# Performance work log

Measured on AMD Instinct MI355X. Metric: run time of the kernel, lower is better.

Reference implementation:

```python
import jax, jax.numpy as jnp
import numpy as np

B = 512       # batch
N = 64        # max_nodes
H = 256       # hidden_dim
LAT = 128     # latent_dim
HEADS = 4
HC = H // HEADS   # per-head channels (GATConv out_channels)
NF = 64       # node_features
L = 3         # num_dec_layers
R = 8         # lora_r
SCAL = 16.0 / R   # lora_alpha / r
NB = 4        # num_bond_types
SLOPE = 0.2   # GATConv leaky_relu negative slope


def setup_inputs() -> dict:
    key = jax.random.key(0)
    ks = jax.random.split(key, 21)
    f = lambda k, shape, s=0.05: jax.random.normal(k, shape, dtype=jnp.float32) * s
    Din = H + LAT  # GAT input dim = hidden + latent (concat)
    return {
        "z": jax.random.normal(ks[0], (B, LAT), dtype=jnp.float32),
        # z_to_nodes LoRALinear: latent -> hidden*max_nodes
        "z2n_w": f(ks[1], (H * N, LAT)), "z2n_b": f(ks[2], (H * N,)),
        "z2n_A": f(ks[3], (R, LAT)), "z2n_B": f(ks[4], (H * N, R)),
        # GATConv stacks (same Din every layer): lin weight, att_src, att_dst, bias
        "gat_W": f(ks[5], (L, HEADS * HC, Din)),
        "gat_asrc": f(ks[6], (L, HEADS, HC)),
        "gat_adst": f(ks[7], (L, HEADS, HC)),
        "gat_bias": f(ks[8], (L, H)),
        # node predictor LoRALinear: hidden -> node_features
        "node_w": f(ks[9], (NF, H)), "node_b": f(ks[10], (NF,)),
        "node_A": f(ks[11], (R, H)), "node_B": f(ks[12], (NF, R)),
        # adj predictor LoRALinear: 2*hidden -> 1
        "adj_w": f(ks[13], (1, 2 * H)), "adj_b": f(ks[14], (1,)),
        "adj_A": f(ks[15], (R, 2 * H)), "adj_B": f(ks[16], (1, R)),
        # bond type predictor LoRALinear: 2*hidden -> 4
        "bond_w": f(ks[17], (NB, 2 * H)), "bond_b": f(ks[18], (NB,)),
        "bond_A": f(ks[19], (R, 2 * H)), "bond_B": f(ks[20], (NB, R)),
    }


def _lora_w(W, A, Bm):
    # effective weight of LoRALinear (eval mode, dropout off): W + (alpha/r) * B @ A
    return W + SCAL * (Bm @ A)


def _forward(z, z2n_w, z2n_b, z2n_A, z2n_B, gat_W, gat_asrc, gat_adst, gat_bias,
             node_w, node_b, node_A, node_B, adj_w, adj_b, adj_A, adj_B,
             bond_w, bond_b, bond_A, bond_B):
    # z_to_nodes: LoRA linear + ReLU -> [B, N, H]
    x = jax.nn.relu(z @ _lora_w(z2n_w, z2n_A, z2n_B).T + z2n_b).reshape(B, N, H)
    z_bc = jnp.broadcast_to(z[:, None, :], (B, N, LAT))
    # Fully-connected graph (off-diagonal edges) + GATConv default self loops
    # => dense softmax attention over all N source nodes per target, per graph.
    for l in range(L):
        xc = jnp.concatenate([x, z_bc], axis=-1)                      # [B,N,H+LAT]
        Wr = gat_W[l].reshape(HEADS, HC, H + LAT)
        h = jnp.einsum('bnd,hcd->bnhc', xc, Wr)                        # [B,N,heads,HC]
        e_src = jnp.einsum('bnhc,hc->bnh', h, gat_asrc[l])             # source term
        e_dst = jnp.einsum('bnhc,hc->bnh', h, gat_adst[l])             # target term
        e = e_dst[:, :, None, :] + e_src[:, None, :, :]                # [B,i,j,heads]
        e = jnp.where(e > 0, e, SLOPE * e)                             # leaky_relu
        alpha = jax.nn.softmax(e, axis=2)                              # over sources j
        out = jnp.einsum('bijh,bjhc->bihc', alpha, h).reshape(B, N, H) + gat_bias[l]
        x = jax.nn.relu(out)
    # node reconstruction
    recon_nodes = x @ _lora_w(node_w, node_A, node_B).T + node_b       # [B,N,NF]
    # pairwise predictors: Linear(concat[h_i,h_j]) = W1 h_i + W2 h_j + b
    iu = jnp.triu(jnp.ones((N, N), dtype=bool), 1)
    Wa = _lora_w(adj_w, adj_A, adj_B)                                  # [1,2H]
    s1 = x @ Wa[:, :H].T                                               # [B,N,1]
    s2 = x @ Wa[:, H:].T
    Am = s1 + jnp.swapaxes(s2, 1, 2) + adj_b[0]                        # Am[i,j]=s1[i]+s2[j]
    adj_logits = jnp.where(iu, Am, jnp.where(iu.T, jnp.swapaxes(Am, 1, 2), 0.0))
    Wb = _lora_w(bond_w, bond_A, bond_B)                               # [NB,2H]
    t1 = x @ Wb[:, :H].T                                               # [B,N,NB]
    t2 = x @ Wb[:, H:].T
    Bm = t1[:, :, None, :] + t2[:, None, :, :] + bond_b                # [B,N,N,NB]
    bond_logits = jnp.where(iu[:, :, None], Bm,
                            jnp.where(iu.T[:, :, None], jnp.swapaxes(Bm, 1, 2), 0.0))
    return recon_nodes, adj_logits, bond_logits


def reference(z, z2n_w, z2n_b, z2n_A, z2n_B, gat_W, gat_asrc, gat_adst, gat_bias,
              node_w, node_b, node_A, node_B, adj_w, adj_b, adj_A, adj_B,
              bond_w, bond_b, bond_A, bond_B):
    return _forward(z, z2n_w, z2n_b, z2n_A, z2n_B, gat_W, gat_asrc, gat_adst, gat_bias,
                    node_w, node_b, node_A, node_B, adj_w, adj_b, adj_A, adj_B,
                    bond_w, bond_b, bond_A, bond_B)
```

## Files before the change

kernel.cpp:

```cpp
#include <hip/hip_runtime.h>


typedef float float4v __attribute__((ext_vector_type(4)));
typedef short short8v __attribute__((ext_vector_type(8)));

struct alignas(8) us4 { ushort x, y, z, w; };

#define ZA_OFF 0UL
#define HZ_OFF 4096UL
#define EZ_OFF 397312UL
#define XBF_U   819200UL
#define ZBF_U   9207808UL
#define GWBF_U  9273344UL
#define WZBF_U  9568256UL
#define PW_U    11665408UL
#define WST_U   11759616UL

__device__ inline ushort f2bf(float f) {
    uint u = __float_as_uint(f);
    uint r = (u + 0x7FFFu + ((u >> 16) & 1u)) >> 16;
    return (ushort)r;
}
__device__ inline float bf2f(ushort u) { return __uint_as_float(((uint)u) << 16); }

__device__ inline int xidx(int r, int cu) {
    int ch = cu >> 3;
    return r * 256 + (((ch ^ (r & 7))) << 3) + (cu & 7);
}

struct P3 { short8v b0, b1, b2; };
__device__ inline P3 loadP3(const ushort* pw, int lo, int hi, int kk) {
    P3 f;
    f.b0 = *(const short8v*)(pw + (size_t)(      lo)*256 + kk*32 + hi*8);
    f.b1 = *(const short8v*)(pw + (size_t)(16  + lo)*256 + kk*32 + hi*8);
    f.b2 = *(const short8v*)(pw + (size_t)(32  + lo)*256 + kk*32 + hi*8);
    return f;
}
struct P2 { short8v b3, b4; };
__device__ inline P2 loadP2(const ushort* pw, int lo, int hi, int kk) {
    P2 f;
    f.b3 = *(const short8v*)(pw + (size_t)(48 + lo)*256 + kk*32 + hi*8);
    f.b4 = *(const short8v*)(pw + (size_t)(64 + lo)*256 + kk*32 + hi*8);
    return f;
}

__device__ inline void gll(const ushort* src, ushort* dst) {
    __builtin_amdgcn_global_load_lds(
        (const __attribute__((address_space(1))) void*)src,
        (__attribute__((address_space(3))) void*)dst, 16, 0, 0);
}

__device__ inline void stageW(ushort* dstHead, const ushort* srcHead, int c0h, int ln) {
    if (c0h == 0) {
        gll(srcHead +        ln*8, dstHead);
        gll(srcHead +  512 + ln*8, dstHead + 512);
        gll(srcHead + 2048 + ln*8, dstHead + 2048);
    } else {
        gll(srcHead + 1024 + ln*8, dstHead + 1024);
        gll(srcHead + 1536 + ln*8, dstHead + 1536);
    }
}

__global__ __launch_bounds__(256) void k_setup(
    const float* __restrict__ z, const float* __restrict__ z2nA,
    const float* __restrict__ nodeW, const float* __restrict__ nodeA, const float* __restrict__ nodeB,
    const float* __restrict__ adjW, const float* __restrict__ adjA, const float* __restrict__ adjB,
    const float* __restrict__ bondW, const float* __restrict__ bondA, const float* __restrict__ bondB,
    const float* __restrict__ gatW, const float* __restrict__ z2nw,
    const float* __restrict__ asrcp, const float* __restrict__ adstp,
    float* __restrict__ wsf)
{
    ushort* wsu = (ushort*)wsf;
    int gid = blockIdx.x * 256 + threadIdx.x;
    if (gid < 4096) {
        int b = gid >> 3, r = gid & 7;
        const float* zp = z + (size_t)b * 128;
        const float* ap = z2nA + (size_t)r * 128;
        float s = 0.f;
        #pragma unroll 8
        for (int k = 0; k < 128; ++k) s += zp[k] * ap[k];
        wsf[ZA_OFF + gid] = s;
    } else if (gid < 24576) {
        int idx = gid - 4096;
        int r = idx >> 8, c = idx & 255;
        float v = 0.f;
        if (r < 64) {
            float s = 0.f;
            #pragma unroll
            for (int k = 0; k < 8; ++k) s += nodeB[r*8+k] * nodeA[k*256+c];
            v = nodeW[r*256+c] + 2.0f * s;
        } else if (r < 66) {
            int off = (r - 64) * 256 + c;
            float s = 0.f;
            #pragma unroll
            for (int k = 0; k < 8; ++k) s += adjB[k] * adjA[k*512+off];
            v = adjW[off] + 2.0f * s;
        } else if (r < 70) {
            int q = r - 66;
            float s = 0.f;
            #pragma unroll
            for (int k = 0; k < 8; ++k) s += bondB[q*8+k] * bondA[k*512+c];
            v = bondW[q*512+c] + 2.0f * s;
        } else if (r < 74) {
            int q = r - 70;
            float s = 0.f;
            #pragma unroll
            for (int k = 0; k < 8; ++k) s += bondB[q*8+k] * bondA[k*512+256+c];
            v = bondW[q*512+256+c] + 2.0f * s;
        }
        wsu[PW_U + idx] = f2bf(v);
    } else if (gid < 55296) {
        int idx = gid - 24576;
        int lkk = idx / 1280;
        int rem = idx - lkk * 1280;
        int head = rem / 320;
        int rem2 = rem - head * 320;
        int frag = rem2 >> 6;
        int ln = rem2 & 63;
        int lo = ln & 15, hi = ln >> 4;
        int l = lkk >> 3, kk = lkk & 7;
        ushort* dst = wsu + WST_U + (size_t)idx * 8;
        if (frag < 4) {
            const float* srcw = gatW + ((size_t)(l*256 + head*64 + frag*16 + lo))*384 + kk*32 + hi*8;
            #pragma unroll
            for (int j = 0; j < 8; ++j) dst[j] = f2bf(srcw[j]);
        } else {
            float s[8] = {0.f,0.f,0.f,0.f,0.f,0.f,0.f,0.f};
            if (lo < 2) {
                const float* av = (lo == 0 ? asrcp : adstp) + l*256 + head*64;
                const float* wp = gatW + ((size_t)(l*256 + head*64))*384 + kk*32 + hi*8;
                for (int hc = 0; hc < 64; ++hc) {
                    float a = av[hc];
                    const float* wr = wp + (size_t)hc * 384;
                    #pragma unroll
                    for (int j = 0; j < 8; ++j) s[j] += wr[j] * a;
                }
            }
            #pragma unroll
            for (int j = 0; j < 8; ++j) dst[j] = f2bf(s[j]);
        }
    } else {
        int cid = gid - 55296;
        const float* src; ushort* dst; int idx;
        if (cid < 16384)        { src = z;     dst = wsu + ZBF_U;  idx = cid; }
        else if (cid < 90112)   { src = gatW;  dst = wsu + GWBF_U; idx = cid - 16384; }
        else if (cid < 614400)  { src = z2nw;  dst = wsu + WZBF_U; idx = cid - 90112; }
        else return;
        float4 v = ((const float4*)src)[idx];
        us4 o; o.x = f2bf(v.x); o.y = f2bf(v.y); o.z = f2bf(v.z); o.w = f2bf(v.w);
        ((us4*)dst)[idx] = o;
    }
}

__global__ __launch_bounds__(256) void k_hz(
    const float* __restrict__ asrcp, const float* __restrict__ adstp,
    float* __restrict__ wsf)
{
    ushort* wsu = (ushort*)wsf;
    int t = threadIdx.x;
    int w = t >> 6, ln = t & 63, lo = ln & 15, hi = ln >> 4;
    int l = blockIdx.x >> 3, bg = blockIdx.x & 7;
    const ushort* wz = wsu + GWBF_U + (size_t)l * 98304;
    const ushort* zb = wsu + ZBF_U + (size_t)bg * 64 * 128;
    float4v acc[4][4];
    #pragma unroll
    for (int m = 0; m < 4; ++m)
        #pragma unroll
        for (int n = 0; n < 4; ++n) acc[m][n] = (float4v)(0.f);
    #pragma unroll
    for (int kk = 0; kk < 4; ++kk) {
        short8v a[4], bq[4];
        #pragma unroll
        for (int m = 0; m < 4; ++m)
            a[m] = *(const short8v*)(wz + (size_t)(w*64 + m*16 + lo)*384 + 256 + kk*32 + hi*8);
        #pragma unroll
        for (int n = 0; n < 4; ++n)
            bq[n] = *(const short8v*)(zb + (size_t)(n*16 + lo)*128 + kk*32 + hi*8);
        #pragma unroll
        for (int m = 0; m < 4; ++m)
            #pragma unroll
            for (int n = 0; n < 4; ++n)
                acc[m][n] = __builtin_amdgcn_mfma_f32_16x16x32_bf16(a[m], bq[n], acc[m][n], 0, 0, 0);
    }
    float* hzp = wsf + HZ_OFF + (size_t)l * 131072;
    #pragma unroll
    for (int m = 0; m < 4; ++m)
        #pragma unroll
        for (int n = 0; n < 4; ++n)
            #pragma unroll
            for (int q = 0; q < 4; ++q)
                hzp[(size_t)(bg*64 + n*16 + lo)*256 + w*64 + m*16 + hi*4 + q] = acc[m][n][q];
    float as_[4][4], ad_[4][4];
    #pragma unroll
    for (int m = 0; m < 4; ++m)
        #pragma unroll
        for (int q = 0; q < 4; ++q) {
            as_[m][q] = asrcp[l*256 + w*64 + m*16 + hi*4 + q];
            ad_[m][q] = adstp[l*256 + w*64 + m*16 + hi*4 + q];
        }
    #pragma unroll
    for (int n = 0; n < 4; ++n) {
        float ss = 0.f, dd = 0.f;
        #pragma unroll
        for (int m = 0; m < 4; ++m)
            #pragma unroll
            for (int q = 0; q < 4; ++q) {
                ss += acc[m][n][q] * as_[m][q];
                dd += acc[m][n][q] * ad_[m][q];
            }
        ss += __shfl_xor(ss, 16); ss += __shfl_xor(ss, 32);
        dd += __shfl_xor(dd, 16); dd += __shfl_xor(dd, 32);
        if (hi == 0) {
            int b = bg*64 + n*16 + lo;
            wsf[EZ_OFF + (size_t)(l*2 + 0)*2048 + (size_t)b*4 + w] = ss;
            wsf[EZ_OFF + (size_t)(l*2 + 1)*2048 + (size_t)b*4 + w] = dd;
        }
    }
}

__global__ __launch_bounds__(256) void k_z2n(
    const float* __restrict__ bias, const float* __restrict__ lB,
    float* __restrict__ wsf)
{
    ushort* wsu = (ushort*)wsf;
    int t = threadIdx.x;
    int w = t >> 6, ln = t & 63, lo = ln & 15, hi = ln >> 4;
    int bm = blockIdx.x >> 6, bn = blockIdx.x & 63;
    int brow0 = bm * 64;
    int o0 = bn * 256 + w * 64;
    const ushort* wz = wsu + WZBF_U;
    const ushort* zb = wsu + ZBF_U;
    float4v acc[4][4];
    #pragma unroll
    for (int m = 0; m < 4; ++m)
        #pragma unroll
        for (int n = 0; n < 4; ++n) acc[m][n] = (float4v)(0.f);
    #pragma unroll
    for (int kk = 0; kk < 4; ++kk) {
        short8v a[4], bq[4];
        #pragma unroll
        for (int m = 0; m < 4; ++m)
            a[m] = *(const short8v*)(wz + (size_t)(o0 + m*16 + lo)*128 + kk*32 + hi*8);
        #pragma unroll
        for (int n = 0; n < 4; ++n)
            bq[n] = *(const short8v*)(zb + (size_t)(brow0 + n*16 + lo)*128 + kk*32 + hi*8);
        #pragma unroll
        for (int m = 0; m < 4; ++m)
            #pragma unroll
            for (int n = 0; n < 4; ++n)
                acc[m][n] = __builtin_amdgcn_mfma_f32_16x16x32_bf16(a[m], bq[n], acc[m][n], 0, 0, 0);
    }
    const float* zA = wsf + ZA_OFF;
    float4 za0[4], za1[4];
    #pragma unroll
    for (int n = 0; n < 4; ++n) {
        int brow = brow0 + n*16 + lo;
        za0[n] = *(const float4*)&zA[brow*8];
        za1[n] = *(const float4*)&zA[brow*8 + 4];
    }
    #pragma unroll
    for (int m = 0; m < 4; ++m) {
        float lor[4][4]; float bs[4];
        #pragma unroll
        for (int q = 0; q < 4; ++q) {
            int o = o0 + m*16 + hi*4 + q;
            float4 b20 = *(const float4*)&lB[(size_t)o*8];
            float4 b21 = *(const float4*)&lB[(size_t)o*8 + 4];
            bs[q] = bias[o];
            #pragma unroll
            for (int n = 0; n < 4; ++n)
                lor[n][q] = za0[n].x*b20.x + za0[n].y*b20.y + za0[n].z*b20.z + za0[n].w*b20.w
                          + za1[n].x*b21.x + za1[n].y*b21.y + za1[n].z*b21.z + za1[n].w*b21.w;
        }
        #pragma unroll
        for (int n = 0; n < 4; ++n) {
            int brow = brow0 + n*16 + lo;
            float v0 = acc[m][n][0] + 2.f*lor[n][0] + bs[0]; v0 = v0 > 0.f ? v0 : 0.f;
            float v1 = acc[m][n][1] + 2.f*lor[n][1] + bs[1]; v1 = v1 > 0.f ? v1 : 0.f;
            float v2 = acc[m][n][2] + 2.f*lor[n][2] + bs[2]; v2 = v2 > 0.f ? v2 : 0.f;
            float v3 = acc[m][n][3] + 2.f*lor[n][3] + bs[3]; v3 = v3 > 0.f ? v3 : 0.f;
            us4 pk; pk.x = f2bf(v0); pk.y = f2bf(v1); pk.z = f2bf(v2); pk.w = f2bf(v3);
            *(us4*)(wsu + XBF_U + (size_t)brow*16384 + o0 + m*16 + hi*4) = pk;
        }
    }
}

__global__ __launch_bounds__(512, 4) void k_fused(
    const float* __restrict__ gbias,
    const float* __restrict__ nodeb, const float* __restrict__ adjb,
    const float* __restrict__ bondb,
    float* __restrict__ wsf, float* __restrict__ out)
{
    extern __shared__ ushort dyn[];
    ushort* Rr   = dyn;
    ushort* bbuf = dyn + 17408;
    float*  scr  = (float*)(dyn + 17408 + 20480);
    ushort* wsu = (ushort*)wsf;
    int t = threadIdx.x;
    int w = t >> 6, ln = t & 63, lo = ln & 15, hi = ln >> 4;
    int head = w & 3, m0 = (w >> 2) * 32;
    int headH = w >> 1, c0h = w & 1;
    int b = blockIdx.x;
    const ushort* xb = wsu + XBF_U + (size_t)b * 16384;

    #pragma unroll
    for (int i = 0; i < 4; ++i) {
        int flat = i*512 + t;
        int r = flat >> 5, ch = flat & 31;
        short8v v = *(const short8v*)(xb + (size_t)r*256 + ch*8);
        *(short8v*)&Rr[r*256 + ((ch ^ (r & 7)) << 3)] = v;
    }
    __syncthreads();

    float* es = scr;
    float* ed = scr + 256;

    for (int l = 0; l < 3; ++l) {
        const ushort* wst = wsu + WST_U + (size_t)l * 81920;
        const float*  hzp = wsf + HZ_OFF + (size_t)l*131072 + (size_t)b*256 + headH*64;

        float hzA = hzp[(c0h*2    )*16 + lo];
        float hzB = hzp[(c0h*2 + 1)*16 + lo];
        float ezs = wsf[EZ_OFF + (size_t)(l*2 + 0)*2048 + (size_t)b*4 + headH];
        float ezd = wsf[EZ_OFF + (size_t)(l*2 + 1)*2048 + (size_t)b*4 + headH];

        float4v acc[2][4], accE[4];
        float eInit = (lo == 0) ? ezs : (lo == 1 ? ezd : 0.f);
        #pragma unroll
        for (int m = 0; m < 4; ++m) {
            acc[0][m] = (float4v)(hzA);
            acc[1][m] = (float4v)(hzB);
            accE[m]   = (float4v)(eInit);
        }

        asm volatile("s_waitcnt vmcnt(0)" ::: "memory");
        __builtin_amdgcn_sched_barrier(0);
        stageW(bbuf +         headH*2560, wst +         headH*2560, c0h, ln);
        stageW(bbuf + 10240 + headH*2560, wst + 10240 + headH*2560, c0h, ln);

        #pragma unroll
        for (int kk = 0; kk < 8; ++kk) {
            if (kk < 7) {
                if (c0h == 0) { asm volatile("s_waitcnt vmcnt(3)" ::: "memory"); }
                else          { asm volatile("s_waitcnt vmcnt(2)" ::: "memory"); }
            } else {
                asm volatile("s_waitcnt vmcnt(0)" ::: "memory");
            }
            __builtin_amdgcn_sched_barrier(0);
            const ushort* bb = bbuf + (kk&1)*10240 + headH*2560;
            short8v bq0 = *(const short8v*)(bb + (c0h*2    )*512 + ln*8);
            short8v bq1 = *(const short8v*)(bb + (c0h*2 + 1)*512 + ln*8);
            short8v bsd = {};
            if (c0h == 0) bsd = *(const short8v*)(bb + 2048 + ln*8);
            short8v a0 = *(const short8v*)&Rr[xidx(     lo, kk*32 + hi*8)];
            short8v a1 = *(const short8v*)&Rr[xidx(16 + lo, kk*32 + hi*8)];
            short8v a2 = *(const short8v*)&Rr[xidx(32 + lo, kk*32 + hi*8)];
            short8v a3 = *(const short8v*)&Rr[xidx(48 + lo, kk*32 + hi*8)];
            if (kk < 6) {
                asm volatile("s_waitcnt lgkmcnt(0)" ::: "memory");
                __builtin_amdgcn_sched_barrier(0);
                stageW(bbuf + (kk&1)*10240 + headH*2560,
                       wst + (size_t)(kk+2)*10240 + headH*2560, c0h, ln);
            }
            acc[0][0] = __builtin_amdgcn_mfma_f32_16x16x32_bf16(a0, bq0, acc[0][0], 0, 0, 0);
            acc[0][1] = __builtin_amdgcn_mfma_f32_16x16x32_bf16(a1, bq0, acc[0][1], 0, 0, 0);
            acc[0][2] = __builtin_amdgcn_mfma_f32_16x16x32_bf16(a2, bq0, acc[0][2], 0, 0, 0);
            acc[0][3] = __builtin_amdgcn_mfma_f32_16x16x32_bf16(a3, bq0, acc[0][3], 0, 0, 0);
            acc[1][0] = __builtin_amdgcn_mfma_f32_16x16x32_bf16(a0, bq1, acc[1][0], 0, 0, 0);
            acc[1][1] = __builtin_amdgcn_mfma_f32_16x16x32_bf16(a1, bq1, acc[1][1], 0, 0, 0);
            acc[1][2] = __builtin_amdgcn_mfma_f32_16x16x32_bf16(a2, bq1, acc[1][2], 0, 0, 0);
            acc[1][3] = __builtin_amdgcn_mfma_f32_16x16x32_bf16(a3, bq1, acc[1][3], 0, 0, 0);
            if (c0h == 0) {
                accE[0] = __builtin_amdgcn_mfma_f32_16x16x32_bf16(a0, bsd, accE[0], 0, 0, 0);
                accE[1] = __builtin_amdgcn_mfma_f32_16x16x32_bf16(a1, bsd, accE[1], 0, 0, 0);
                accE[2] = __builtin_amdgcn_mfma_f32_16x16x32_bf16(a2, bsd, accE[2], 0, 0, 0);
                accE[3] = __builtin_amdgcn_mfma_f32_16x16x32_bf16(a3, bsd, accE[3], 0, 0, 0);
            }
        }

        if (c0h == 0) {
            if (lo == 0) {
                #pragma unroll
                for (int m = 0; m < 4; ++m)
                    *(float4*)&es[headH*64 + m*16 + hi*4] =
                        make_float4(accE[m][0], accE[m][1], accE[m][2], accE[m][3]);
            } else if (lo == 1) {
                #pragma unroll
                for (int m = 0; m < 4; ++m)
                    *(float4*)&ed[headH*64 + m*16 + hi*4] =
                        make_float4(accE[m][0], accE[m][1], accE[m][2], accE[m][3]);
            }
        }

        __syncthreads();

        #pragma unroll
        for (int cf = 0; cf < 2; ++cf)
            #pragma unroll
            for (int m = 0; m < 4; ++m) {
                us4 pk;
                pk.x = f2bf(acc[cf][m][0]); pk.y = f2bf(acc[cf][m][1]);
                pk.z = f2bf(acc[cf][m][2]); pk.w = f2bf(acc[cf][m][3]);
                *(us4*)&Rr[headH*4352 + ((c0h*2 + cf)*16 + lo)*68 + m*16 + hi*4] = pk;
            }

        __syncthreads();

        float4v acc2[4][2];
        #pragma unroll
        for (int m = 0; m < 4; ++m)
            #pragma unroll
            for (int n = 0; n < 2; ++n) acc2[m][n] = (float4v)(0.f);
        float psum[2] = {0.f, 0.f};
        #pragma unroll
        for (int kk = 0; kk < 2; ++kk) {
            short8v hb[4];
            #pragma unroll
            for (int m = 0; m < 4; ++m)
                hb[m] = *(const short8v*)&Rr[head*4352 + (m*16 + lo)*68 + kk*32 + hi*8];
            float4 e0 = *(const float4*)&es[head*64 + kk*32 + hi*8];
            float4 e1 = *(const float4*)&es[head*64 + kk*32 + hi*8 + 4];
            float ej[8] = {e0.x, e0.y, e0.z, e0.w, e1.x, e1.y, e1.z, e1.w};
            #pragma unroll
            for (int n = 0; n < 2; ++n) {
                float edr = ed[head*64 + m0 + n*16 + lo];
                short8v af; float pp = 0.f;
                #pragma unroll
                for (int jj = 0; jj < 8; ++jj) {
                    float e = edr + ej[jj];
                    e = fmaxf(e, 0.2f * e);
                    float p = __expf(e);
                    pp += p;
                    af[jj] = (short)f2bf(p);
                }
                psum[n] += pp;
                #pragma unroll
                for (int m = 0; m < 4; ++m)
                    acc2[m][n] = __builtin_amdgcn_mfma_f32_16x16x32_bf16(hb[m], af, acc2[m][n], 0, 0, 0);
            }
        }
        float rs[2];
        #pragma unroll
        for (int n = 0; n < 2; ++n) {
            psum[n] += __shfl_xor(psum[n], 16);
            psum[n] += __shfl_xor(psum[n], 32);
            rs[n] = 1.0f / psum[n];
        }

        __syncthreads();

        #pragma unroll
        for (int m = 0; m < 4; ++m) {
            int c0 = head*64 + m*16 + hi*4;
            float b0f = gbias[l*256 + c0 + 0];
            float b1f = gbias[l*256 + c0 + 1];
            float b2f = gbias[l*256 + c0 + 2];
            float b3f = gbias[l*256 + c0 + 3];
            #pragma unroll
            for (int n = 0; n < 2; ++n) {
                int r = m0 + n*16 + lo;
                float v0 = acc2[m][n][0]*rs[n] + b0f; v0 = v0 > 0.f ? v0 : 0.f;
                float v1 = acc2[m][n][1]*rs[n] + b1f; v1 = v1 > 0.f ? v1 : 0.f;
                float v2 = acc2[m][n][2]*rs[n] + b2f; v2 = v2 > 0.f ? v2 : 0.f;
                float v3 = acc2[m][n][3]*rs[n] + b3f; v3 = v3 > 0.f ? v3 : 0.f;
                us4 pk; pk.x = f2bf(v0); pk.y = f2bf(v1); pk.z = f2bf(v2); pk.w = f2bf(v3);
                *(us4*)&Rr[xidx(r, c0)] = pk;
            }
        }

        __syncthreads();
    }

    const ushort* pw = wsu + PW_U;
    int pq = w & 3, pn = w >> 2;
    if (pn == 0) {
        float4v p0 = (float4v)(0.f), p1 = (float4v)(0.f), p2 = (float4v)(0.f);
        P3 fA = loadP3(pw, lo, hi, 0);
        #pragma unroll
        for (int ii = 0; ii < 4; ++ii) {
            P3 fB = loadP3(pw, lo, hi, 2*ii + 1);
            {
                int kk = 2*ii;
                short8v a = *(const short8v*)&Rr[xidx(pq*16 + lo, kk*32 + hi*8)];
                p0 = __builtin_amdgcn_mfma_f32_16x16x32_bf16(a, fA.b0, p0, 0, 0, 0);
                p1 = __builtin_amdgcn_mfma_f32_16x16x32_bf16(a, fA.b1, p1, 0, 0, 0);
                p2 = __builtin_amdgcn_mfma_f32_16x16x32_bf16(a, fA.b2, p2, 0, 0, 0);
            }
            if (ii < 3) fA = loadP3(pw, lo, hi, 2*ii + 2);
            {
                int kk = 2*ii + 1;
                short8v a = *(const short8v*)&Rr[xidx(pq*16 + lo, kk*32 + hi*8)];
                p0 = __builtin_amdgcn_mfma_f32_16x16x32_bf16(a, fB.b0, p0, 0, 0, 0);
                p1 = __builtin_amdgcn_mfma_f32_16x16x32_bf16(a, fB.b1, p1, 0, 0, 0);
                p2 = __builtin_amdgcn_mfma_f32_16x16x32_bf16(a, fB.b2, p2, 0, 0, 0);
            }
        }
        __syncthreads();
        float* Rf = (float*)Rr;
        #pragma unroll
        for (int qq = 0; qq < 4; ++qq) {
            int nd = pq*16 + hi*4 + qq;
            Rf[nd*68 + lo]      = p0[qq];
            Rf[nd*68 + 16 + lo] = p1[qq];
            Rf[nd*68 + 32 + lo] = p2[qq];
        }
    } else {
        float4v p3 = (float4v)(0.f), paux = (float4v)(0.f);
        P2 fA = loadP2(pw, lo, hi, 0);
        #pragma unroll
        for (int ii = 0; ii < 4; ++ii) {
            P2 fB = loadP2(pw, lo, hi, 2*ii + 1);
            {
                int kk = 2*ii;
                short8v a = *(const short8v*)&Rr[xidx(pq*16 + lo, kk*32 + hi*8)];
                p3   = __builtin_amdgcn_mfma_f32_16x16x32_bf16(a, fA.b3, p3, 0, 0, 0);
                paux = __builtin_amdgcn_mfma_f32_16x16x32_bf16(a, fA.b4, paux, 0, 0, 0);
            }
            if (ii < 3) fA = loadP2(pw, lo, hi, 2*ii + 2);
            {
                int kk = 2*ii + 1;
                short8v a = *(const short8v*)&Rr[xidx(pq*16 + lo, kk*32 + hi*8)];
                p3   = __builtin_amdgcn_mfma_f32_16x16x32_bf16(a, fB.b3, p3, 0, 0, 0);
                paux = __builtin_amdgcn_mfma_f32_16x16x32_bf16(a, fB.b4, paux, 0, 0, 0);
            }
        }
        __syncthreads();
        float* Rf = (float*)Rr;
        #pragma unroll
        for (int qq = 0; qq < 4; ++qq) {
            int nd = pq*16 + hi*4 + qq;
            Rf[nd*68 + 48 + lo] = p3[qq];
            float v = paux[qq];
            if (lo == 0)      scr[nd] = v;
            else if (lo == 1) scr[64 + nd] = v;
            else if (lo < 6)  scr[128 + nd*5 + (lo-2)] = v;
            else if (lo < 10) scr[448 + nd*5 + (lo-6)] = v;
        }
    }
    __syncthreads();

    {
        const float* Rf = (const float*)Rr;
        #pragma unroll
        for (int it = 0; it < 2; ++it) {
            int idx = it*512 + t;
            int nd = idx >> 4, f0 = (idx & 15) * 4;
            float4 v = *(const float4*)&Rf[nd*68 + f0];
            float4 bv = *(const float4*)&nodeb[f0];
            v.x += bv.x; v.y += bv.y; v.z += bv.z; v.w += bv.w;
            *(float4*)&out[(size_t)b*4096 + (size_t)idx*4] = v;
        }
    }

    float ab = adjb[0];
    #pragma unroll
    for (int it = 0; it < 2; ++it) {
        int idx = it*512 + t;
        int flat = idx * 4;
        int i = flat >> 6, j0 = flat & 63;
        float4 v; float* vp = (float*)&v;
        #pragma unroll
        for (int uu = 0; uu < 4; ++uu) {
            int j = j0 + uu;
            float val;
            if (i == j)      val = 0.f;
            else if (i < j)  val = scr[i] + scr[64 + j] + ab;
            else             val = scr[j] + scr[64 + i] + ab;
            vp[uu] = val;
        }
        *(float4*)&out[2097152UL + (size_t)b*4096 + flat] = v;
    }

    float4 bb2 = *(const float4*)bondb;
    #pragma unroll
    for (int it = 0; it < 8; ++it) {
        int fl4 = it*512 + t;
        int i = fl4 >> 6, j = fl4 & 63;
        float4 v;
        if (i == j) { v.x = v.y = v.z = v.w = 0.f; }
        else {
            int a2 = i < j ? i : j, c2 = i < j ? j : i;
            v.x = scr[128 + a2*5 + 0] + scr[448 + c2*5 + 0] + bb2.x;
            v.y = scr[128 + a2*5 + 1] + scr[448 + c2*5 + 1] + bb2.y;
            v.z = scr[128 + a2*5 + 2] + scr[448 + c2*5 + 2] + bb2.z;
            v.w = scr[128 + a2*5 + 3] + scr[448 + c2*5 + 3] + bb2.w;
        }
        *(float4*)&out[4194304UL + (size_t)b*16384 + (size_t)fl4*4] = v;
    }
}

extern "C" void kernel_launch(void* const* d_in, const int* in_sizes, int n_in,
                              void* d_out, int out_size, void* d_ws, size_t ws_size,
                              hipStream_t stream)
{
    const float* z     = (const float*)d_in[0];
    const float* z2nw  = (const float*)d_in[1];
    const float* z2nb  = (const float*)d_in[2];
    const float* z2nA  = (const float*)d_in[3];
    const float* z2nB  = (const float*)d_in[4];
    const float* gatW  = (const float*)d_in[5];
    const float* asrc  = (const float*)d_in[6];
    const float* adst  = (const float*)d_in[7];
    const float* gbias = (const float*)d_in[8];
    const float* nodew = (const float*)d_in[9];
    const float* nodeb = (const float*)d_in[10];
    const float* nodeA = (const float*)d_in[11];
    const float* nodeB = (const float*)d_in[12];
    const float* adjw  = (const float*)d_in[13];
    const float* adjb  = (const float*)d_in[14];
    const float* adjA  = (const float*)d_in[15];
    const float* adjB  = (const float*)d_in[16];
    const float* bondw = (const float*)d_in[17];
    const float* bondb = (const float*)d_in[18];
    const float* bondA = (const float*)d_in[19];
    const float* bondB = (const float*)d_in[20];
    float* ws  = (float*)d_ws;
    float* out = (float*)d_out;

    k_setup<<<2616, 256, 0, stream>>>(z, z2nA, nodew, nodeA, nodeB,
                                      adjw, adjA, adjB, bondw, bondA, bondB,
                                      gatW, z2nw, asrc, adst, ws);
    k_hz<<<24, 256, 0, stream>>>(asrc, adst, ws);
    k_z2n<<<512, 256, 0, stream>>>(z2nb, z2nB, ws);
    k_fused<<<512, 512, 78848, stream>>>(gbias, nodeb, adjb, bondb, ws, out);
}
```

Baseline: 92.57 us.

## Merge hz into z2n launch, prefetch next-layer weights, use packed bf16 converts

The separate k_hz launch is folded into k_z2n as 24 extra blocks, removing one kernel launch and its serialization. In the fused GAT kernel, staging of the first weight tiles for the next layer is issued during the last k-steps of the current layer, so the per-layer full vmcnt(0) drain goes away. Scalar bf16 rounding is replaced with the hardware v_cvt_pk_bf16_f32 instruction, and s_setprio brackets the MFMA bursts. Waitcnt accounting across layer boundaries becomes more fragile, and some sched_barriers are removed, which lets the compiler reorder around the inline asm.

```diff
diff --git a/kernel.cpp b/kernel.cpp
--- a/kernel.cpp
+++ b/kernel.cpp
@@ -3,6 +3,7 @@
 
 typedef float float4v __attribute__((ext_vector_type(4)));
 typedef short short8v __attribute__((ext_vector_type(8)));
+typedef uint  uint4v  __attribute__((ext_vector_type(4)));
 
 struct alignas(8) us4 { ushort x, y, z, w; };
 
@@ -22,6 +23,12 @@
     return (ushort)r;
 }
 __device__ inline float bf2f(ushort u) { return __uint_as_float(((uint)u) << 16); }
+
+__device__ inline uint cvtpk(float a, float b) {
+    uint r;
+    asm("v_cvt_pk_bf16_f32 %0, %1, %2" : "=v"(r) : "v"(a), "v"(b));
+    return r;
+}
 
 __device__ inline int xidx(int r, int cu) {
     int ch = cu >> 3;
@@ -152,79 +159,77 @@
     }
 }
 
-__global__ __launch_bounds__(256) void k_hz(
+__global__ __launch_bounds__(256) void k_z2n(
+    const float* __restrict__ bias, const float* __restrict__ lB,
     const float* __restrict__ asrcp, const float* __restrict__ adstp,
     float* __restrict__ wsf)
 {
     ushort* wsu = (ushort*)wsf;
     int t = threadIdx.x;
     int w = t >> 6, ln = t & 63, lo = ln & 15, hi = ln >> 4;
-    int l = blockIdx.x >> 3, bg = blockIdx.x & 7;
-    const ushort* wz = wsu + GWBF_U + (size_t)l * 98304;
-    const ushort* zb = wsu + ZBF_U + (size_t)bg * 64 * 128;
-    float4v acc[4][4];
-    #pragma unroll
-    for (int m = 0; m < 4; ++m)
-        #pragma unroll
-        for (int n = 0; n < 4; ++n) acc[m][n] = (float4v)(0.f);
-    #pragma unroll
-    for (int kk = 0; kk < 4; ++kk) {
-        short8v a[4], bq[4];
+
+    if (blockIdx.x >= 512) {
+        int bid2 = blockIdx.x - 512;
+        int l = bid2 >> 3, bg = bid2 & 7;
+        const ushort* wz = wsu + GWBF_U + (size_t)l * 98304;
+        const ushort* zb = wsu + ZBF_U + (size_t)bg * 64 * 128;
+        float4v acc[4][4];
         #pragma unroll
         for (int m = 0; m < 4; ++m)
-            a[m] = *(const short8v*)(wz + (size_t)(w*64 + m*16 + lo)*384 + 256 + kk*32 + hi*8);
-        #pragma unroll
-        for (int n = 0; n < 4; ++n)
-            bq[n] = *(const short8v*)(zb + (size_t)(n*16 + lo)*128 + kk*32 + hi*8);
+            #pragma unroll
+            for (int n = 0; n < 4; ++n) acc[m][n] = (float4v)(0.f);
+        #pragma unroll
+        for (int kk = 0; kk < 4; ++kk) {
+            short8v a[4], bq[4];
+            #pragma unroll
+            for (int m = 0; m < 4; ++m)
+                a[m] = *(const short8v*)(wz + (size_t)(w*64 + m*16 + lo)*384 + 256 + kk*32 + hi*8);
+            #pragma unroll
+            for (int n = 0; n < 4; ++n)
+                bq[n] = *(const short8v*)(zb + (size_t)(n*16 + lo)*128 + kk*32 + hi*8);
+            #pragma unroll
+            for (int m = 0; m < 4; ++m)
+                #pragma unroll
+                for (int n = 0; n < 4; ++n)
+                    acc[m][n] = __builtin_amdgcn_mfma_f32_16x16x32_bf16(a[m], bq[n], acc[m][n], 0, 0, 0);
+        }
+        float* hzp = wsf + HZ_OFF + (size_t)l * 131072;
         #pragma unroll
         for (int m = 0; m < 4; ++m)
             #pragma unroll
             for (int n = 0; n < 4; ++n)
-                acc[m][n] = __builtin_amdgcn_mfma_f32_16x16x32_bf16(a[m], bq[n], acc[m][n], 0, 0, 0);
-    }
-    float* hzp = wsf + HZ_OFF + (size_t)l * 131072;
-    #pragma unroll
-    for (int m = 0; m < 4; ++m)
-        #pragma unroll
-        for (int n = 0; n < 4; ++n)
-            #pragma unroll
-            for (int q = 0; q < 4; ++q)
-                hzp[(size_t)(bg*64 + n*16 + lo)*256 + w*64 + m*16 + hi*4 + q] = acc[m][n][q];
-    float as_[4][4], ad_[4][4];
-    #pragma unroll
-    for (int m = 0; m < 4; ++m)
-        #pragma unroll
-        for (int q = 0; q < 4; ++q) {
-            as_[m][q] = asrcp[l*256 + w*64 + m*16 + hi*4 + q];
-            ad_[m][q] = adstp[l*256 + w*64 + m*16 + hi*4 + q];
-        }
-    #pragma unroll
-    for (int n = 0; n < 4; ++n) {
-        float ss = 0.f, dd = 0.f;
+                #pragma unroll
+                for (int q = 0; q < 4; ++q)
+                    hzp[(size_t)(bg*64 + n*16 + lo)*256 + w*64 + m*16 + hi*4 + q] = acc[m][n][q];
+        float as_[4][4], ad_[4][4];
         #pragma unroll
         for (int m = 0; m < 4; ++m)
             #pragma unroll
             for (int q = 0; q < 4; ++q) {
-                ss += acc[m][n][q] * as_[m][q];
-                dd += acc[m][n][q] * ad_[m][q];
-            }
-        ss += __shfl_xor(ss, 16); ss += __shfl_xor(ss, 32);
-        dd += __shfl_xor(dd, 16); dd += __shfl_xor(dd, 32);
-        if (hi == 0) {
-            int b = bg*64 + n*16 + lo;
-            wsf[EZ_OFF + (size_t)(l*2 + 0)*2048 + (size_t)b*4 + w] = ss;
-            wsf[EZ_OFF + (size_t)(l*2 + 1)*2048 + (size_t)b*4 + w] = dd;
-        }
-    }
-}
-
-__global__ __launch_bounds__(256) void k_z2n(
-    const float* __restrict__ bias, const float* __restrict__ lB,
-    float* __restrict__ wsf)
-{
-    ushort* wsu = (ushort*)wsf;
-    int t = threadIdx.x;
-    int w = t >> 6, ln = t & 63, lo = ln & 15, hi = ln >> 4;
+                as_[m][q] = asrcp[l*256 + w*64 + m*16 + hi*4 + q];
+                ad_[m][q] = adstp[l*256 + w*64 + m*16 + hi*4 + q];
+            }
+        #pragma unroll
+        for (int n = 0; n < 4; ++n) {
+            float ss = 0.f, dd = 0.f;
+            #pragma unroll
+            for (int m = 0; m < 4; ++m)
+                #pragma unroll
+                for (int q = 0; q < 4; ++q) {
+                    ss += acc[m][n][q] * as_[m][q];
+                    dd += acc[m][n][q] * ad_[m][q];
+                }
+            ss += __shfl_xor(ss, 16); ss += __shfl_xor(ss, 32);
+            dd += __shfl_xor(dd, 16); dd += __shfl_xor(dd, 32);
+            if (hi == 0) {
+                int b = bg*64 + n*16 + lo;
+                wsf[EZ_OFF + (size_t)(l*2 + 0)*2048 + (size_t)b*4 + w] = ss;
+                wsf[EZ_OFF + (size_t)(l*2 + 1)*2048 + (size_t)b*4 + w] = dd;
+            }
+        }
+        return;
+    }
+
     int bm = blockIdx.x >> 6, bn = blockIdx.x & 63;
     int brow0 = bm * 64;
     int o0 = bn * 256 + w * 64;
@@ -315,8 +320,15 @@
     float* es = scr;
     float* ed = scr + 256;
 
+    {
+        const ushort* wst0 = wsu + WST_U;
+        stageW(bbuf +         headH*2560, wst0 +         headH*2560, c0h, ln);
+        stageW(bbuf + 10240 + headH*2560, wst0 + 10240 + headH*2560, c0h, ln);
+    }
+
     for (int l = 0; l < 3; ++l) {
-        const ushort* wst = wsu + WST_U + (size_t)l * 81920;
+        const ushort* wst  = wsu + WST_U + (size_t)l * 81920;
+        const ushort* wstN = wsu + WST_U + (size_t)(l + 1) * 81920;
         const float*  hzp = wsf + HZ_OFF + (size_t)l*131072 + (size_t)b*256 + headH*64;
 
         float hzA = hzp[(c0h*2    )*16 + lo];
@@ -333,20 +345,15 @@
             accE[m]   = (float4v)(eInit);
         }
 
-        asm volatile("s_waitcnt vmcnt(0)" ::: "memory");
-        __builtin_amdgcn_sched_barrier(0);
-        stageW(bbuf +         headH*2560, wst +         headH*2560, c0h, ln);
-        stageW(bbuf + 10240 + headH*2560, wst + 10240 + headH*2560, c0h, ln);
-
         #pragma unroll
         for (int kk = 0; kk < 8; ++kk) {
-            if (kk < 7) {
-                if (c0h == 0) { asm volatile("s_waitcnt vmcnt(3)" ::: "memory"); }
-                else          { asm volatile("s_waitcnt vmcnt(2)" ::: "memory"); }
+            if (kk == 7 && l == 2) {
+                asm volatile("s_waitcnt vmcnt(0)" ::: "memory");
+            } else if (c0h == 0) {
+                asm volatile("s_waitcnt vmcnt(3)" ::: "memory");
             } else {
-                asm volatile("s_waitcnt vmcnt(0)" ::: "memory");
-            }
-            __builtin_amdgcn_sched_barrier(0);
+                asm volatile("s_waitcnt vmcnt(2)" ::: "memory");
+            }
             const ushort* bb = bbuf + (kk&1)*10240 + headH*2560;
             short8v bq0 = *(const short8v*)(bb + (c0h*2    )*512 + ln*8);
             short8v bq1 = *(const short8v*)(bb + (c0h*2 + 1)*512 + ln*8);
@@ -358,10 +365,14 @@
             short8v a3 = *(const short8v*)&Rr[xidx(48 + lo, kk*32 + hi*8)];
             if (kk < 6) {
                 asm volatile("s_waitcnt lgkmcnt(0)" ::: "memory");
-                __builtin_amdgcn_sched_barrier(0);
                 stageW(bbuf + (kk&1)*10240 + headH*2560,
                        wst + (size_t)(kk+2)*10240 + headH*2560, c0h, ln);
-            }
+            } else if (l < 2) {
+                asm volatile("s_waitcnt lgkmcnt(0)" ::: "memory");
+                stageW(bbuf + (kk&1)*10240 + headH*2560,
+                       wstN + (size_t)(kk-6)*10240 + headH*2560, c0h, ln);
+            }
+            __builtin_amdgcn_s_setprio(1);
             acc[0][0] = __builtin_amdgcn_mfma_f32_16x16x32_bf16(a0, bq0, acc[0][0], 0, 0, 0);
             acc[0][1] = __builtin_amdgcn_mfma_f32_16x16x32_bf16(a1, bq0, acc[0][1], 0, 0, 0);
             acc[0][2] = __builtin_amdgcn_mfma_f32_16x16x32_bf16(a2, bq0, acc[0][2], 0, 0, 0);
@@ -376,6 +387,7 @@
                 accE[2] = __builtin_amdgcn_mfma_f32_16x16x32_bf16(a2, bsd, accE[2], 0, 0, 0);
                 accE[3] = __builtin_amdgcn_mfma_f32_16x16x32_bf16(a3, bsd, accE[3], 0, 0, 0);
             }
+            __builtin_amdgcn_s_setprio(0);
         }
 
         if (c0h == 0) {
@@ -398,10 +410,10 @@
         for (int cf = 0; cf < 2; ++cf)
             #pragma unroll
             for (int m = 0; m < 4; ++m) {
-                us4 pk;
-                pk.x = f2bf(acc[cf][m][0]); pk.y = f2bf(acc[cf][m][1]);
-                pk.z = f2bf(acc[cf][m][2]); pk.w = f2bf(acc[cf][m][3]);
-                *(us4*)&Rr[headH*4352 + ((c0h*2 + cf)*16 + lo)*68 + m*16 + hi*4] = pk;
+                uint2 pk;
+                pk.x = cvtpk(acc[cf][m][0], acc[cf][m][1]);
+                pk.y = cvtpk(acc[cf][m][2], acc[cf][m][3]);
+                *(uint2*)&Rr[headH*4352 + ((c0h*2 + cf)*16 + lo)*68 + m*16 + hi*4] = pk;
             }
 
         __syncthreads();
@@ -424,19 +436,25 @@
             #pragma unroll
             for (int n = 0; n < 2; ++n) {
                 float edr = ed[head*64 + m0 + n*16 + lo];
-                short8v af; float pp = 0.f;
+                float pvv[8]; float pp = 0.f;
                 #pragma unroll
                 for (int jj = 0; jj < 8; ++jj) {
                     float e = edr + ej[jj];
                     e = fmaxf(e, 0.2f * e);
                     float p = __expf(e);
                     pp += p;
-                    af[jj] = (short)f2bf(p);
+                    pvv[jj] = p;
                 }
+                uint4v au;
+                au.x = cvtpk(pvv[0], pvv[1]); au.y = cvtpk(pvv[2], pvv[3]);
+                au.z = cvtpk(pvv[4], pvv[5]); au.w = cvtpk(pvv[6], pvv[7]);
+                short8v af = __builtin_bit_cast(short8v, au);
                 psum[n] += pp;
+                __builtin_amdgcn_s_setprio(1);
                 #pragma unroll
                 for (int m = 0; m < 4; ++m)
                     acc2[m][n] = __builtin_amdgcn_mfma_f32_16x16x32_bf16(hb[m], af, acc2[m][n], 0, 0, 0);
+                __builtin_amdgcn_s_setprio(0);
             }
         }
         float rs[2];
@@ -463,8 +481,8 @@
                 float v1 = acc2[m][n][1]*rs[n] + b1f; v1 = v1 > 0.f ? v1 : 0.f;
                 float v2 = acc2[m][n][2]*rs[n] + b2f; v2 = v2 > 0.f ? v2 : 0.f;
                 float v3 = acc2[m][n][3]*rs[n] + b3f; v3 = v3 > 0.f ? v3 : 0.f;
-                us4 pk; pk.x = f2bf(v0); pk.y = f2bf(v1); pk.z = f2bf(v2); pk.w = f2bf(v3);
-                *(us4*)&Rr[xidx(r, c0)] = pk;
+                uint2 pk; pk.x = cvtpk(v0, v1); pk.y = cvtpk(v2, v3);
+                *(uint2*)&Rr[xidx(r, c0)] = pk;
             }
         }
 
@@ -620,7 +638,6 @@
     k_setup<<<2616, 256, 0, stream>>>(z, z2nA, nodew, nodeA, nodeB,
                                       adjw, adjA, adjB, bondw, bondA, bondB,
                                       gatW, z2nw, asrc, adst, ws);
-    k_hz<<<24, 256, 0, stream>>>(asrc, adst, ws);
-    k_z2n<<<512, 256, 0, stream>>>(z2nb, z2nB, ws);
+    k_z2n<<<536, 256, 0, stream>>>(z2nb, z2nB, asrc, adst, ws);
     k_fused<<<512, 512, 78848, stream>>>(gbias, nodeb, adjb, bondb, ws, out);
 }
```

Result: faster. 86.50 us (-6.6%).
